# Optimization experiments

Hardware: AMD Instinct MI355X
Metric: run time of the kernel (lower is better)

## Reference

```python
import jax, jax.numpy as jnp
import numpy as np

V, E, H = 2048, 256, 256
B, T, MMAX = 256, 16, 96  # blocks, max tokens/instr, max instrs/block


def setup_inputs() -> dict:
    key = jax.random.key(0)
    ks = jax.random.split(key, 13)
    # instruction lengths sorted descending (enforce_sorted=True), 96 down to 33
    instr_lens = (96 - (np.arange(B) * 64) // B).astype(np.int64)
    boundaries = np.concatenate([[0], np.cumsum(instr_lens)]).astype(np.int64)
    N = int(boundaries[-1])  # total instructions = 16512
    padded_tokens = jax.random.randint(ks[0], (N, T), 1, V)
    token_lengths = jax.random.randint(ks[1], (N,), 1, T + 1)
    tmask = jnp.arange(T)[None, :] < token_lengths[:, None]
    padded_tokens = jnp.where(tmask, padded_tokens, 0)  # pad with padding_idx=0
    s = 1.0 / np.sqrt(H)
    def u(k, shape):
        return jax.random.uniform(k, shape, jnp.float32, -s, s)
    emb = u(ks[2], (V, E)).at[0].set(0.0)  # padding_idx row is zero
    return dict(
        padded_tokens=padded_tokens.astype(jnp.int64),
        token_lengths=token_lengths.astype(jnp.int64),
        instruction_lengths=jnp.asarray(instr_lens),
        instr_boundaries=jnp.asarray(boundaries),
        embedding=emb,
        w_ih_tok=u(ks[3], (4 * H, E)), w_hh_tok=u(ks[4], (4 * H, H)),
        b_ih_tok=u(ks[5], (4 * H,)), b_hh_tok=u(ks[6], (4 * H,)),
        w_ih_ins=u(ks[7], (4 * H, H)), w_hh_ins=u(ks[8], (4 * H, H)),
        b_ih_ins=u(ks[9], (4 * H,)), b_hh_ins=u(ks[10], (4 * H,)),
        w_lin=u(ks[11], (1, H)), b_lin=u(ks[12], (1,)),
    )


def _lstm_final(x, lengths, w_ih, w_hh, b_ih, b_hh):
    # x: [N, S, D] padded; returns hidden state at last valid step per sequence [N, H]
    N, S, _ = x.shape
    Hh = w_hh.shape[1]
    mask = jnp.arange(S)[:, None] < lengths[None, :]  # [S, N]
    bias = b_ih + b_hh

    def step(carry, inp):
        h, c = carry
        x_t, m = inp  # x_t: [N, D], m: [N]
        g = x_t @ w_ih.T + h @ w_hh.T + bias  # [N, 4H], PyTorch gate order i,f,g,o
        i, f, gg, o = jnp.split(g, 4, axis=-1)
        c_new = jax.nn.sigmoid(f) * c + jax.nn.sigmoid(i) * jnp.tanh(gg)
        h_new = jax.nn.sigmoid(o) * jnp.tanh(c_new)
        m = m[:, None]
        return (jnp.where(m, h_new, h), jnp.where(m, c_new, c)), None

    h0 = jnp.zeros((N, Hh), x.dtype)
    (h, _), _ = jax.lax.scan(step, (h0, h0), (jnp.swapaxes(x, 0, 1), mask))
    return h


def reference(padded_tokens, token_lengths, instruction_lengths, instr_boundaries,
              embedding, w_ih_tok, w_hh_tok, b_ih_tok, b_hh_tok,
              w_ih_ins, w_hh_ins, b_ih_ins, b_hh_ins, w_lin, b_lin):
    # token-level LSTM over all instructions (packed == masked scan)
    emb_tokens = embedding[padded_tokens]  # [N, T, E]
    instr_inputs = _lstm_final(emb_tokens, token_lengths,
                               w_ih_tok, w_hh_tok, b_ih_tok, b_hh_tok)  # [N, H]
    N = instr_inputs.shape[0]
    # regroup instructions into blocks via boundaries (pad_sequence equivalent)
    idx = instr_boundaries[:-1, None] + jnp.arange(MMAX)[None, :]  # [B, MMAX]
    valid = jnp.arange(MMAX)[None, :] < instruction_lengths[:, None]
    gathered = jnp.where(valid[..., None],
                         instr_inputs[jnp.clip(idx, 0, N - 1)], 0.0)  # [B, MMAX, H]
    final = _lstm_final(gathered, instruction_lengths,
                        w_ih_ins, w_hh_ins, b_ih_ins, b_hh_ins)  # [B, H]
    return (final @ w_lin.T + b_lin).squeeze(-1)  # [B]
```

## Files before the change

### kernel.cpp

```cpp
#include <hip/hip_runtime.h>
#include <hip/hip_bf16.h>
#include <math.h>

#define VSZ 2048
#define EDIM 256
#define HDIM 256
#define G4 1024
#define TMAX 16
#define IB 16

typedef _Float16 f16x2 __attribute__((ext_vector_type(2)));
typedef _Float16 f16x4 __attribute__((ext_vector_type(4)));
typedef _Float16 f16x8 __attribute__((ext_vector_type(8)));
typedef float f32x4 __attribute__((ext_vector_type(4)));

#define HA_STRIDE 264
#define GWH_STRIDE 264

__device__ __forceinline__ float fexp2(float x) {
#if defined(__has_builtin) && __has_builtin(__builtin_amdgcn_exp2f)
  return __builtin_amdgcn_exp2f(x);
#else
  return exp2f(x);
#endif
}
__device__ __forceinline__ float frcp(float x) {
#if defined(__has_builtin) && __has_builtin(__builtin_amdgcn_rcpf)
  return __builtin_amdgcn_rcpf(x);
#else
  return 1.0f / x;
#endif
}
__device__ __forceinline__ float sigm(float x) {
  return frcp(1.0f + fexp2(x * -1.44269504f));
}
__device__ __forceinline__ float tanh_fast(float x) {
  float t = fexp2(fminf(x, 15.0f) * 2.88539008f);
  return (t - 1.0f) * frcp(t + 1.0f);
}

__device__ __forceinline__ float fdot2(f16x2 a, f16x2 b, float c) {
#if defined(__has_builtin) && __has_builtin(__builtin_amdgcn_fdot2)
  return __builtin_amdgcn_fdot2(a, b, c, false);
#else
  return c + (float)a.x * (float)b.x + (float)a.y * (float)b.y;
#endif
}

__device__ __forceinline__ float dot8h(uint4 w, float4 hv, float acc) {
  f16x2 h0 = __builtin_bit_cast(f16x2, hv.x);
  f16x2 h1 = __builtin_bit_cast(f16x2, hv.y);
  f16x2 h2 = __builtin_bit_cast(f16x2, hv.z);
  f16x2 h3 = __builtin_bit_cast(f16x2, hv.w);
  f16x2 w0 = __builtin_bit_cast(f16x2, w.x);
  f16x2 w1 = __builtin_bit_cast(f16x2, w.y);
  f16x2 w2 = __builtin_bit_cast(f16x2, w.z);
  f16x2 w3 = __builtin_bit_cast(f16x2, w.w);
  return fdot2(h3, w3, fdot2(h2, w2, fdot2(h1, w1, fdot2(h0, w0, acc))));
}

__device__ __forceinline__ bool is_f32(const void* w) {
  const unsigned short* p = (const unsigned short*)w;
  int pl = 0;
#pragma unroll
  for (int i = 0; i < 64; ++i) {
    unsigned e = (p[2 * i] >> 7) & 0xFF;
    pl += (e >= 113 && e <= 122) ? 1 : 0;
  }
  return pl < 48;
}

template <bool F32>
__device__ __forceinline__ float ldf(const void* p, long j) {
  if (F32) return ((const float*)p)[j];
  return __uint_as_float(((unsigned)((const unsigned short*)p)[j]) << 16);
}
__device__ __forceinline__ float ldf_rt(const void* p, long j, bool f32) {
  if (f32) return ((const float*)p)[j];
  return __uint_as_float(((unsigned)((const unsigned short*)p)[j]) << 16);
}
template <bool I64>
__device__ __forceinline__ int ldi(const int* p, int j) {
  return I64 ? p[2 * j] : p[j];
}
__device__ __forceinline__ int ldi_rt(const int* p, int j, bool i64) {
  return i64 ? p[2 * j] : p[j];
}

__global__ __launch_bounds__(256) void k_transp(const void* src, float* __restrict__ dst,
                                                const void* fprobe) {
  __shared__ float tile[32][33];
  __shared__ int sf;
  if (threadIdx.x == 0) sf = is_f32(fprobe) ? 1 : 0;
  __syncthreads();
  const bool f32 = (sf != 0);
  const int tx = threadIdx.x & 31, ty = threadIdx.x >> 5;
  const int r0 = blockIdx.x * 32, c0 = blockIdx.y * 32;
#pragma unroll
  for (int q = 0; q < 4; ++q) {
    int rr = ty + q * 8;
    tile[rr][tx] = ldf_rt(src, (long)(r0 + rr) * 256 + (c0 + tx), f32);
  }
  __syncthreads();
#pragma unroll
  for (int q = 0; q < 4; ++q) {
    int cc = ty + q * 8;
    dst[(size_t)(c0 + cc) * 1024 + (r0 + tx)] = tile[tx][cc];
  }
}

__global__ __launch_bounds__(256) void k_pack(const void* src, uint4* __restrict__ dst,
                                              const void* fprobe) {
  __shared__ int sf;
  if (threadIdx.x == 0) sf = is_f32(fprobe) ? 1 : 0;
  __syncthreads();
  const bool f32 = (sf != 0);
  const int idx = blockIdx.x * 256 + threadIdx.x;
  const int rr = idx & 255, j = (idx >> 8) & 3, c = idx >> 10;
  const long base = (long)(j * 256 + rr) * 256 + 8 * c;
  unsigned u[4];
#pragma unroll
  for (int q = 0; q < 4; ++q) {
    f16x2 v;
    v.x = (_Float16)ldf_rt(src, base + 2 * q, f32);
    v.y = (_Float16)ldf_rt(src, base + 2 * q + 1, f32);
    u[q] = __builtin_bit_cast(unsigned, v);
  }
  uint4 o; o.x = u[0]; o.y = u[1]; o.z = u[2]; o.w = u[3];
  dst[idx] = o;
}

__global__ __launch_bounds__(256) void k_packB(const void* src, f16x8* __restrict__ dst,
                                               const void* fprobe) {
  __shared__ int sf;
  if (threadIdx.x == 0) sf = is_f32(fprobe) ? 1 : 0;
  __syncthreads();
  const bool f32 = (sf != 0);
  const int idx = blockIdx.x * 256 + threadIdx.x;
  const int l = idx & 63;
  int rest = idx >> 6;
  const int kt = rest & 7; rest >>= 3;
  const int nt = rest & 15;
  const int w = rest >> 4;
  const int n = 256 * w + nt * 16 + (l & 15);
  const int j = n & 3, e = n >> 2;
  const long base = (long)(j * 256 + e) * 256 + kt * 32 + ((l >> 4) << 3);
  f16x8 v;
#pragma unroll
  for (int q = 0; q < 8; ++q) v[q] = (_Float16)ldf_rt(src, base + q, f32);
  dst[idx] = v;
}

template <bool F32>
__device__ void tok_table_impl(const void* emb, const float* __restrict__ wT,
                               const void* bih, const void* bhh,
                               f16x4* __restrict__ tabi4, float (*xs)[256]) {
  const int t = threadIdx.x;
  const int v0 = blockIdx.x * 16;
#pragma unroll
  for (int i = 0; i < 16; ++i) xs[i][t] = ldf<F32>(emb, (long)(v0 + i) * EDIM + t);
  __syncthreads();
  float acc[4][16];
#pragma unroll
  for (int j = 0; j < 4; ++j)
#pragma unroll
    for (int i = 0; i < 16; ++i) acc[j][i] = 0.f;
  for (int k4 = 0; k4 < 64; ++k4) {
    float w[4][4];
#pragma unroll
    for (int kk = 0; kk < 4; ++kk)
#pragma unroll
      for (int j = 0; j < 4; ++j)
        w[j][kk] = wT[(size_t)(k4 * 4 + kk) * 1024 + j * 256 + t];
#pragma unroll
    for (int i = 0; i < 16; ++i) {
      float4 h4 = *(const float4*)&xs[i][k4 * 4];
#pragma unroll
      for (int j = 0; j < 4; ++j)
        acc[j][i] = fmaf(h4.x, w[j][0], fmaf(h4.y, w[j][1],
                    fmaf(h4.z, w[j][2], fmaf(h4.w, w[j][3], acc[j][i]))));
    }
  }
  float b[4];
#pragma unroll
  for (int j = 0; j < 4; ++j)
    b[j] = ldf<F32>(bih, j * 256 + t) + ldf<F32>(bhh, j * 256 + t);
#pragma unroll
  for (int i = 0; i < 16; ++i) {
    f16x4 v;
    v.x = (_Float16)(acc[0][i] + b[0]);
    v.y = (_Float16)(acc[1][i] + b[1]);
    v.z = (_Float16)(acc[2][i] + b[2]);
    v.w = (_Float16)(acc[3][i] + b[3]);
    tabi4[(size_t)(v0 + i) * 256 + t] = v;
  }
}

__global__ __launch_bounds__(256) void k_tok_table(
    const void* emb, const float* __restrict__ wT, const void* bih,
    const void* bhh, f16x4* __restrict__ tabi4, const void* fprobe) {
  __shared__ float xs[16][256];
  __shared__ int sf;
  if (threadIdx.x == 0) sf = is_f32(fprobe) ? 1 : 0;
  __syncthreads();
  if (sf) tok_table_impl<true>(emb, wT, bih, bhh, tabi4, xs);
  else    tok_table_impl<false>(emb, wT, bih, bhh, tabi4, xs);
}

__global__ __launch_bounds__(1024) void k_bucket(const int* tlen, int N,
                                                 int* __restrict__ perm,
                                                 const int* iprobe) {
  __shared__ int cnt[16][18];
  __shared__ int wbase[16][18];
  __shared__ int base[18];
  const int t = threadIdx.x;
  const int w = t >> 6;
  const bool i64 = (iprobe[1] == 0);
  if (t < 16 * 18) ((int*)cnt)[t] = 0;
  __syncthreads();
  for (int n = t; n < N; n += 1024) {
    int len = ldi_rt(tlen, n, i64);
    len = max(0, min(16, len));
    atomicAdd(&cnt[w][len], 1);
  }
  __syncthreads();
  if (t < 17) {
    int s = 0;
    for (int ww = 0; ww < 16; ++ww) { wbase[ww][t] = s; s += cnt[ww][t]; }
    base[t] = s;
  }
  __syncthreads();
  if (t == 0) {
    int s = 0;
    for (int i = 0; i <= 16; ++i) { int c = base[i]; base[i] = s; s += c; }
  }
  __syncthreads();
  if (t < 16 * 18) ((int*)cnt)[t] = 0;
  __syncthreads();
  for (int n = t; n < N; n += 1024) {
    int len = ldi_rt(tlen, n, i64);
    len = max(0, min(16, len));
    int pos = base[len] + wbase[w][len] + atomicAdd(&cnt[w][len], 1);
    perm[pos] = n;
  }
}

struct TokSmemM {
  _Float16 gateW[4][16 * GWH_STRIDE];
  _Float16 hA[16 * HA_STRIDE];
  int tokL[IB][TMAX];
  int lenL[IB];
  int nIdx[IB];
};

template <bool I64>
__device__ void tok_mfma_impl(const int* tok32, const int* tlen32,
                              const int* __restrict__ perm,
                              const f16x4* __restrict__ tabi4,
                              const f16x8* __restrict__ pkB,
                              const f16x8* __restrict__ pkBI,
                              const void* bihI, const void* bhhI,
                              float* __restrict__ instrH, float* __restrict__ gx,
                              int N, int do_gx, bool f32, TokSmemM& sm) {
  const int n0 = blockIdx.x * IB, t = threadIdx.x;
  const int w = t >> 6, l = t & 63;
  if (t < IB) {
    int slot = n0 + t;
    int n = (slot < N) ? perm[slot] : -1;
    sm.nIdx[t] = n;
    sm.lenL[t] = (n >= 0) ? ldi<I64>(tlen32, n) : 0;
  }
  for (int idx = t; idx < 16 * HA_STRIDE / 2; idx += 256) ((unsigned*)sm.hA)[idx] = 0;
  __syncthreads();
  {
    int i = t >> 4, s = t & 15;
    int n = sm.nIdx[i];
    sm.tokL[i][s] = (n >= 0) ? ldi<I64>(tok32, n * TMAX + s) : 0;
  }
  float c[IB];
#pragma unroll
  for (int i = 0; i < IB; ++i) c[i] = 0.f;
  __syncthreads();
  int maxlen = 0;
#pragma unroll
  for (int i = 0; i < IB; ++i) maxlen = max(maxlen, sm.lenL[i]);

  const f16x8* Bp = pkB + (size_t)w * (16 * 8 * 64);
  const int aOff = (l & 15) * HA_STRIDE + ((l >> 4) << 3);
  const int m0 = (l >> 4) << 2;
  _Float16* gw = sm.gateW[w];

  for (int s = 0; s < maxlen; ++s) {
    f16x8 aF[8];
#pragma unroll
    for (int kt = 0; kt < 8; ++kt)
      aF[kt] = *(const f16x8*)&sm.hA[aOff + kt * 32];
#pragma unroll 2
    for (int g4 = 0; g4 < 4; ++g4) {
      f32x4 a0 = {0.f, 0.f, 0.f, 0.f}, a1 = a0, a2 = a0, a3 = a0;
#pragma unroll
      for (int kt = 0; kt < 8; ++kt) {
        const f16x8* bb = Bp + ((size_t)(g4 * 4) * 8 + kt) * 64 + l;
        f16x8 b0 = bb[0 * 8 * 64];
        f16x8 b1 = bb[1 * 8 * 64];
        f16x8 b2 = bb[2 * 8 * 64];
        f16x8 b3 = bb[3 * 8 * 64];
        a0 = __builtin_amdgcn_mfma_f32_16x16x32_f16(aF[kt], b0, a0, 0, 0, 0);
        a1 = __builtin_amdgcn_mfma_f32_16x16x32_f16(aF[kt], b1, a1, 0, 0, 0);
        a2 = __builtin_amdgcn_mfma_f32_16x16x32_f16(aF[kt], b2, a2, 0, 0, 0);
        a3 = __builtin_amdgcn_mfma_f32_16x16x32_f16(aF[kt], b3, a3, 0, 0, 0);
      }
      const int colb = (l & 15);
#pragma unroll
      for (int r = 0; r < 4; ++r) {
        gw[(m0 + r) * GWH_STRIDE + (g4 * 4 + 0) * 16 + colb] = (_Float16)a0[r];
        gw[(m0 + r) * GWH_STRIDE + (g4 * 4 + 1) * 16 + colb] = (_Float16)a1[r];
        gw[(m0 + r) * GWH_STRIDE + (g4 * 4 + 2) * 16 + colb] = (_Float16)a2[r];
        gw[(m0 + r) * GWH_STRIDE + (g4 * 4 + 3) * 16 + colb] = (_Float16)a3[r];
      }
    }
    __syncthreads();
#pragma unroll
    for (int m = 0; m < IB; ++m) {
      if (s < sm.lenL[m]) {
        f16x4 gv = *(const f16x4*)&gw[m * GWH_STRIDE + 4 * l];
        f16x4 tb = tabi4[(size_t)sm.tokL[m][s] * 256 + t];
        float gi = (float)gv.x + (float)tb.x;
        float gf = (float)gv.y + (float)tb.y;
        float gg = (float)gv.z + (float)tb.z;
        float go = (float)gv.w + (float)tb.w;
        float si = sigm(gi), sf = sigm(gf), tg = tanh_fast(gg), so = sigm(go);
        c[m] = sf * c[m] + si * tg;
        sm.hA[m * HA_STRIDE + t] = (_Float16)(so * tanh_fast(c[m]));
      }
    }
    __syncthreads();
  }
#pragma unroll
  for (int m = 0; m < IB; ++m) {
    int n = sm.nIdx[m];
    if (n >= 0) instrH[(size_t)n * HDIM + t] = (float)sm.hA[m * HA_STRIDE + t];
  }
  if (do_gx) {
    f16x8 aF[8];
#pragma unroll
    for (int kt = 0; kt < 8; ++kt)
      aF[kt] = *(const f16x8*)&sm.hA[aOff + kt * 32];
    const f16x8* BpI = pkBI + (size_t)w * (16 * 8 * 64);
#pragma unroll 2
    for (int g4 = 0; g4 < 4; ++g4) {
      f32x4 a0 = {0.f, 0.f, 0.f, 0.f}, a1 = a0, a2 = a0, a3 = a0;
#pragma unroll
      for (int kt = 0; kt < 8; ++kt) {
        const f16x8* bb = BpI + ((size_t)(g4 * 4) * 8 + kt) * 64 + l;
        f16x8 b0 = bb[0 * 8 * 64];
        f16x8 b1 = bb[1 * 8 * 64];
        f16x8 b2 = bb[2 * 8 * 64];
        f16x8 b3 = bb[3 * 8 * 64];
        a0 = __builtin_amdgcn_mfma_f32_16x16x32_f16(aF[kt], b0, a0, 0, 0, 0);
        a1 = __builtin_amdgcn_mfma_f32_16x16x32_f16(aF[kt], b1, a1, 0, 0, 0);
        a2 = __builtin_amdgcn_mfma_f32_16x16x32_f16(aF[kt], b2, a2, 0, 0, 0);
        a3 = __builtin_amdgcn_mfma_f32_16x16x32_f16(aF[kt], b3, a3, 0, 0, 0);
      }
      const int colb = (l & 15);
#pragma unroll
      for (int r = 0; r < 4; ++r) {
        gw[(m0 + r) * GWH_STRIDE + (g4 * 4 + 0) * 16 + colb] = (_Float16)a0[r];
        gw[(m0 + r) * GWH_STRIDE + (g4 * 4 + 1) * 16 + colb] = (_Float16)a1[r];
        gw[(m0 + r) * GWH_STRIDE + (g4 * 4 + 2) * 16 + colb] = (_Float16)a2[r];
        gw[(m0 + r) * GWH_STRIDE + (g4 * 4 + 3) * 16 + colb] = (_Float16)a3[r];
      }
    }
    __syncthreads();
    const float bj0 = ldf_rt(bihI, 0 * 256 + t, f32) + ldf_rt(bhhI, 0 * 256 + t, f32);
    const float bj1 = ldf_rt(bihI, 1 * 256 + t, f32) + ldf_rt(bhhI, 1 * 256 + t, f32);
    const float bj2 = ldf_rt(bihI, 2 * 256 + t, f32) + ldf_rt(bhhI, 2 * 256 + t, f32);
    const float bj3 = ldf_rt(bihI, 3 * 256 + t, f32) + ldf_rt(bhhI, 3 * 256 + t, f32);
#pragma unroll
    for (int m = 0; m < IB; ++m) {
      int n = sm.nIdx[m];
      if (n >= 0) {
        f16x4 gv = *(const f16x4*)&gw[m * GWH_STRIDE + 4 * l];
        gx[(size_t)n * G4 +       t] = (float)gv.x + bj0;
        gx[(size_t)n * G4 + 256 + t] = (float)gv.y + bj1;
        gx[(size_t)n * G4 + 512 + t] = (float)gv.z + bj2;
        gx[(size_t)n * G4 + 768 + t] = (float)gv.w + bj3;
      }
    }
  }
}

__global__ __launch_bounds__(256, 2) void k_tok_lstm(
    const int* tok32, const int* tlen32, const int* __restrict__ perm,
    const f16x4* __restrict__ tabi4, const f16x8* __restrict__ pkB,
    const f16x8* __restrict__ pkBI, const void* bihI, const void* bhhI,
    float* __restrict__ instrH, float* __restrict__ gx, int N, int do_gx,
    const int* iprobe, const void* fprobe) {
  __shared__ TokSmemM sm;
  __shared__ int sfl;
  if (threadIdx.x == 0)
    sfl = ((iprobe[1] == 0) ? 1 : 0) | (is_f32(fprobe) ? 2 : 0);
  __syncthreads();
  const bool f32 = (sfl & 2) != 0;
  if (sfl & 1) tok_mfma_impl<true >(tok32, tlen32, perm, tabi4, pkB, pkBI, bihI, bhhI, instrH, gx, N, do_gx, f32, sm);
  else         tok_mfma_impl<false>(tok32, tlen32, perm, tabi4, pkB, pkBI, bihI, bhhI, instrH, gx, N, do_gx, f32, sm);
}

#define RCH 24
#define LCH 8
struct InsSmem {
  uint4 wL[LCH][1024];
  float gL[1024];
  f16x2 hL2[128];
  float red[256];
};

template <bool F32, bool I64>
__device__ void ins_rec_impl(const int* ilen32, const int* bnd32,
                             const float* __restrict__ gx,
                             const uint4* __restrict__ pk,
                             const void* wlin, const void* blin,
                             float* __restrict__ out, int B, InsSmem& sm) {
  const int b = blockIdx.x, t = threadIdx.x;
  const int j = t >> 8, rr = t & 255;
  const int len = ldi<I64>(ilen32, b);
  const long n0 = (long)ldi<I64>(bnd32, b);
#pragma unroll
  for (int cc = 0; cc < LCH; ++cc)
    sm.wL[cc][t] = pk[((RCH + cc) * 4 + j) * 256 + rr];
  uint4 wr[RCH];
#pragma unroll
  for (int cg = 0; cg < RCH; ++cg)
    wr[cg] = pk[(cg * 4 + j) * 256 + rr];
  if (t < 128) {
    f16x2 z; z.x = (_Float16)0.f; z.y = (_Float16)0.f;
    sm.hL2[t] = z;
  }
  float c = 0.f, h = 0.f;
  __syncthreads();

  for (int m = 0; m < len; ++m) {
    float g0 = 0.f, g1 = 0.f, g2 = 0.f, g3 = 0.f;
    if (t < 256) {
      const float* gp = gx + (size_t)(n0 + m) * G4;
      g0 = gp[t]; g1 = gp[256 + t]; g2 = gp[512 + t]; g3 = gp[768 + t];
    }
    float a0 = 0.f, a1 = 0.f;
#pragma unroll
    for (int cg = 0; cg < RCH; ++cg) {
      float4 hv = ((const float4*)sm.hL2)[cg];
      if (cg & 1) a1 = dot8h(wr[cg], hv, a1);
      else        a0 = dot8h(wr[cg], hv, a0);
    }
#pragma unroll
    for (int cc = 0; cc < LCH; ++cc) {
      float4 hv = ((const float4*)sm.hL2)[RCH + cc];
      if (cc & 1) a1 = dot8h(sm.wL[cc][t], hv, a1);
      else        a0 = dot8h(sm.wL[cc][t], hv, a0);
    }
    sm.gL[t] = a0 + a1;
    __syncthreads();
    if (t < 256) {
      float gi = g0 + sm.gL[t];
      float gf = g1 + sm.gL[256 + t];
      float gg = g2 + sm.gL[512 + t];
      float go = g3 + sm.gL[768 + t];
      float si = sigm(gi), sf = sigm(gf), tg = tanh_fast(gg), so = sigm(go);
      c = sf * c + si * tg;
      h = so * tanh_fast(c);
      ((_Float16*)sm.hL2)[t] = (_Float16)h;
    }
    __syncthreads();
  }
  if (t < 256) sm.red[t] = h * ldf<F32>(wlin, t);
  __syncthreads();
  for (int st = 128; st > 0; st >>= 1) {
    if (t < st) sm.red[t] += sm.red[t + st];
    __syncthreads();
  }
  if (t == 0) out[b] = sm.red[0] + ldf<F32>(blin, 0);
}

__global__ __launch_bounds__(1024) void k_ins_rec(
    const int* ilen32, const int* bnd32, const float* __restrict__ gx,
    const uint4* __restrict__ pk, const void* wlin, const void* blin,
    float* __restrict__ out, int B, const void* fprobe, const int* iprobe) {
  __shared__ InsSmem sm;
  __shared__ int sfl;
  if (threadIdx.x == 0)
    sfl = (is_f32(fprobe) ? 1 : 0) | ((iprobe[1] == 0) ? 2 : 0);
  __syncthreads();
  const int fl = sfl;
  if (fl == 0)      ins_rec_impl<false, false>(ilen32, bnd32, gx, pk, wlin, blin, out, B, sm);
  else if (fl == 1) ins_rec_impl<true,  false>(ilen32, bnd32, gx, pk, wlin, blin, out, B, sm);
  else if (fl == 2) ins_rec_impl<false, true >(ilen32, bnd32, gx, pk, wlin, blin, out, B, sm);
  else              ins_rec_impl<true,  true >(ilen32, bnd32, gx, pk, wlin, blin, out, B, sm);
}

#define IBB 4
struct InsSmemFB {
  float hL[IBB][HDIM];
  float xL[IBB][HDIM];
  float gL[IBB][G4];
};

template <bool F32, bool I64>
__device__ void ins_fb_impl(const int* ilen32, const int* bnd32,
                            const float* __restrict__ instrH,
                            const float* __restrict__ wTih,
                            const float* __restrict__ wThh,
                            const void* bih, const void* bhh,
                            const void* wlin, const void* blin,
                            float* __restrict__ out, int B, InsSmemFB& sm) {
  const int wg = blockIdx.x, t = threadIdx.x;
  const int myblk = t >> 8, myelem = t & 255;
  int len[IBB], n0[IBB];
#pragma unroll
  for (int i = 0; i < IBB; ++i) {
    int b = wg * IBB + i;
    len[i] = (b < B) ? ldi<I64>(ilen32, b) : 0;
    n0[i]  = (b < B) ? ldi<I64>(bnd32, b) : 0;
  }
  float c = 0.f;
  sm.hL[myblk][myelem] = 0.f;
  float bias_r = ldf<F32>(bih, t) + ldf<F32>(bhh, t);
  __syncthreads();
  int maxlen = 0;
#pragma unroll
  for (int i = 0; i < IBB; ++i) maxlen = max(maxlen, len[i]);
  for (int m = 0; m < maxlen; ++m) {
    unsigned act = 0;
#pragma unroll
    for (int i = 0; i < IBB; ++i) if (m < len[i]) act |= (1u << i);
    if (m < len[myblk])
      sm.xL[myblk][myelem] = instrH[(size_t)(n0[myblk] + m) * HDIM + myelem];
    __syncthreads();
    float a[IBB];
#pragma unroll
    for (int i = 0; i < IBB; ++i) a[i] = (act & (1u << i)) ? bias_r : 0.f;
    for (int k4 = 0; k4 < 64; ++k4) {
      float w0 = wThh[(size_t)(k4 * 4 + 0) * 1024 + t];
      float w1 = wThh[(size_t)(k4 * 4 + 1) * 1024 + t];
      float w2 = wThh[(size_t)(k4 * 4 + 2) * 1024 + t];
      float w3 = wThh[(size_t)(k4 * 4 + 3) * 1024 + t];
      float u0 = wTih[(size_t)(k4 * 4 + 0) * 1024 + t];
      float u1 = wTih[(size_t)(k4 * 4 + 1) * 1024 + t];
      float u2 = wTih[(size_t)(k4 * 4 + 2) * 1024 + t];
      float u3 = wTih[(size_t)(k4 * 4 + 3) * 1024 + t];
#pragma unroll
      for (int i = 0; i < IBB; ++i) {
        if (!(act & (1u << i))) continue;
        float4 h4 = *(const float4*)&sm.hL[i][k4 * 4];
        float4 x4 = *(const float4*)&sm.xL[i][k4 * 4];
        a[i] = fmaf(h4.x, w0, fmaf(h4.y, w1, fmaf(h4.z, w2, fmaf(h4.w, w3, a[i]))));
        a[i] = fmaf(x4.x, u0, fmaf(x4.y, u1, fmaf(x4.z, u2, fmaf(x4.w, u3, a[i]))));
      }
    }
#pragma unroll
    for (int i = 0; i < IBB; ++i)
      if (act & (1u << i)) sm.gL[i][t] = a[i];
    __syncthreads();
    if (m < len[myblk]) {
      float si = sigm(sm.gL[myblk][myelem]);
      float sf = sigm(sm.gL[myblk][256 + myelem]);
      float tg = tanh_fast(sm.gL[myblk][512 + myelem]);
      float so = sigm(sm.gL[myblk][768 + myelem]);
      c = sf * c + si * tg;
      sm.hL[myblk][myelem] = so * tanh_fast(c);
    }
    __syncthreads();
  }
  sm.gL[myblk][myelem] = sm.hL[myblk][myelem] * ldf<F32>(wlin, myelem);
  __syncthreads();
  for (int st = 128; st > 0; st >>= 1) {
    if (myelem < st) sm.gL[myblk][myelem] += sm.gL[myblk][myelem + st];
    __syncthreads();
  }
  if (myelem == 0 && wg * IBB + myblk < B)
    out[wg * IBB + myblk] = sm.gL[myblk][0] + ldf<F32>(blin, 0);
}

__global__ __launch_bounds__(1024) void k_ins_fb(
    const int* ilen32, const int* bnd32, const float* __restrict__ instrH,
    const float* __restrict__ wTih, const float* __restrict__ wThh,
    const void* bih, const void* bhh, const void* wlin, const void* blin,
    float* __restrict__ out, int B, const void* fprobe, const int* iprobe) {
  __shared__ InsSmemFB sm;
  __shared__ int sfl;
  if (threadIdx.x == 0)
    sfl = (is_f32(fprobe) ? 1 : 0) | ((iprobe[1] == 0) ? 2 : 0);
  __syncthreads();
  const int fl = sfl;
  if (fl == 0)      ins_fb_impl<false, false>(ilen32, bnd32, instrH, wTih, wThh, bih, bhh, wlin, blin, out, B, sm);
  else if (fl == 1) ins_fb_impl<true,  false>(ilen32, bnd32, instrH, wTih, wThh, bih, bhh, wlin, blin, out, B, sm);
  else if (fl == 2) ins_fb_impl<false, true >(ilen32, bnd32, instrH, wTih, wThh, bih, bhh, wlin, blin, out, B, sm);
  else              ins_fb_impl<true,  true >(ilen32, bnd32, instrH, wTih, wThh, bih, bhh, wlin, blin, out, B, sm);
}

extern "C" void kernel_launch(void* const* d_in, const int* in_sizes, int n_in,
                              void* d_out, int out_size, void* d_ws, size_t ws_size,
                              hipStream_t stream) {
  const int N = in_sizes[1];
  const int B = in_sizes[2];

  float* ws = (float*)d_ws;
  size_t off = 0;
  f16x4* tabi4 = (f16x4*)(ws + off); off += (size_t)VSZ * G4 / 2;
  float* instrH   = ws + off; off += (size_t)N * HDIM;
  float* wT_ihI   = ws + off; off += 262144;
  float* wT_hhI   = ws + off; off += 262144;
  float* wT_ihT   = ws + off; off += 262144;
  f16x8* pkB_tok  = (f16x8*)(ws + off); off += 131072;
  f16x8* pkB_ins  = (f16x8*)(ws + off); off += 131072;
  uint4* pk_ins   = (uint4*)(ws + off); off += 131072;
  int*   permI    = (int*)(ws + off);
  off += ((size_t)N + 15) & ~(size_t)15;
  float* gx       = ws + off;
  const size_t need_gx = (off + (size_t)N * G4) * sizeof(float);
  const bool has_gx = (ws_size >= need_gx);

  const void* fprobe = d_in[5];
  const int*  iprobe = (const int*)d_in[1];

  hipLaunchKernelGGL(k_transp, dim3(32, 8), dim3(256), 0, stream, d_in[5], wT_ihT, fprobe);
  hipLaunchKernelGGL(k_transp, dim3(32, 8), dim3(256), 0, stream, d_in[9], wT_ihI, fprobe);
  hipLaunchKernelGGL(k_transp, dim3(32, 8), dim3(256), 0, stream, d_in[10], wT_hhI, fprobe);
  hipLaunchKernelGGL(k_packB, dim3(128), dim3(256), 0, stream, d_in[6], pkB_tok, fprobe);
  hipLaunchKernelGGL(k_packB, dim3(128), dim3(256), 0, stream, d_in[9], pkB_ins, fprobe);
  hipLaunchKernelGGL(k_pack, dim3(128), dim3(256), 0, stream, d_in[10], pk_ins, fprobe);

  hipLaunchKernelGGL(k_tok_table, dim3(VSZ / 16), dim3(256), 0, stream,
                     d_in[4], wT_ihT, d_in[7], d_in[8], tabi4, fprobe);
  hipLaunchKernelGGL(k_bucket, dim3(1), dim3(1024), 0, stream,
                     (const int*)d_in[1], N, permI, iprobe);
  hipLaunchKernelGGL(k_tok_lstm, dim3((N + IB - 1) / IB), dim3(256), 0, stream,
                     (const int*)d_in[0], (const int*)d_in[1], permI, tabi4,
                     pkB_tok, pkB_ins, d_in[11], d_in[12], instrH, gx, N,
                     has_gx ? 1 : 0, iprobe, fprobe);
  if (has_gx) {
    hipLaunchKernelGGL(k_ins_rec, dim3(B), dim3(1024), 0, stream,
                       (const int*)d_in[2], (const int*)d_in[3], gx, pk_ins,
                       d_in[13], d_in[14], (float*)d_out, B, fprobe, iprobe);
  } else {
    hipLaunchKernelGGL(k_ins_fb, dim3((B + IBB - 1) / IBB), dim3(1024), 0, stream,
                       (const int*)d_in[2], (const int*)d_in[3], instrH,
                       wT_ihI, wT_hhI, d_in[11], d_in[12], d_in[13], d_in[14],
                       (float*)d_out, B, fprobe, iprobe);
  }
}
```

Baseline: 688.9 us.

## Make token LSTM gate elementwise wave-local, removing mid-step barrier

Each wave now processes gate outputs for its own 64 hidden units in two 32-wide halves. It applies the LSTM cell update straight from its private gate buffer, so the intra-step __syncthreads between the MFMA and the elementwise phase is no longer needed. The gate scratch buffer shrinks to half-width per wave and token ids are stored as 16-bit, which cuts shared memory use. The cost is that each thread now holds 16 cell states in a different lane mapping. Interleaving the halves with sched_barrier is meant to overlap MFMA and transcendental work, but it may raise register pressure.

Measured after the change: 1.449 ms. 2.1x slower.

```diff
diff --git a/kernel.cpp b/kernel.cpp
--- a/kernel.cpp
+++ b/kernel.cpp
@@ -15,7 +15,7 @@
 typedef float f32x4 __attribute__((ext_vector_type(4)));
 
 #define HA_STRIDE 264
-#define GWH_STRIDE 264
+#define GH_STRIDE 132
 
 __device__ __forceinline__ float fexp2(float x) {
 #if defined(__has_builtin) && __has_builtin(__builtin_amdgcn_exp2f)
@@ -246,9 +246,9 @@
 }
 
 struct TokSmemM {
-  _Float16 gateW[4][16 * GWH_STRIDE];
+  _Float16 gw4[4][16 * GH_STRIDE];
   _Float16 hA[16 * HA_STRIDE];
-  int tokL[IB][TMAX];
+  unsigned short tokL[IB][TMAX];
   int lenL[IB];
   int nIdx[IB];
 };
@@ -275,7 +275,7 @@
   {
     int i = t >> 4, s = t & 15;
     int n = sm.nIdx[i];
-    sm.tokL[i][s] = (n >= 0) ? ldi<I64>(tok32, n * TMAX + s) : 0;
+    sm.tokL[i][s] = (unsigned short)((n >= 0) ? ldi<I64>(tok32, n * TMAX + s) : 0);
   }
   float c[IB];
 #pragma unroll
@@ -288,58 +288,89 @@
   const f16x8* Bp = pkB + (size_t)w * (16 * 8 * 64);
   const int aOff = (l & 15) * HA_STRIDE + ((l >> 4) << 3);
   const int m0 = (l >> 4) << 2;
-  _Float16* gw = sm.gateW[w];
+  const int colb = l & 15;
+  const int eh = l & 31;
+  const int rp = l >> 5;
+  _Float16* gwq = sm.gw4[w];
+
+#define HALF_MFMA(GH, BASEP)                                                          \
+  {                                                                                   \
+    f32x4 a0 = {0.f, 0.f, 0.f, 0.f}, a1 = a0, a2 = a0, a3 = a0;                       \
+    _Pragma("unroll") for (int kt = 0; kt < 8; ++kt) {                                \
+      const f16x8* bb = BASEP + ((size_t)((GH) * 4) * 8 + kt) * 64 + l;               \
+      f16x8 b0 = bb[0 * 8 * 64];                                                      \
+      f16x8 b1 = bb[1 * 8 * 64];                                                      \
+      f16x8 b2 = bb[2 * 8 * 64];                                                      \
+      f16x8 b3 = bb[3 * 8 * 64];                                                      \
+      a0 = __builtin_amdgcn_mfma_f32_16x16x32_f16(aF[kt], b0, a0, 0, 0, 0);           \
+      a1 = __builtin_amdgcn_mfma_f32_16x16x32_f16(aF[kt], b1, a1, 0, 0, 0);           \
+      a2 = __builtin_amdgcn_mfma_f32_16x16x32_f16(aF[kt], b2, a2, 0, 0, 0);           \
+      a3 = __builtin_amdgcn_mfma_f32_16x16x32_f16(aF[kt], b3, a3, 0, 0, 0);           \
+    }                                                                                 \
+    const int cb = ((GH) & 1) * 64 + colb;                                            \
+    _Pragma("unroll") for (int r = 0; r < 4; ++r) {                                   \
+      gwq[(m0 + r) * GH_STRIDE + cb + 0 * 16] = (_Float16)a0[r];                      \
+      gwq[(m0 + r) * GH_STRIDE + cb + 1 * 16] = (_Float16)a1[r];                      \
+      gwq[(m0 + r) * GH_STRIDE + cb + 2 * 16] = (_Float16)a2[r];                      \
+      gwq[(m0 + r) * GH_STRIDE + cb + 3 * 16] = (_Float16)a3[r];                      \
+    }                                                                                 \
+  }
 
   for (int s = 0; s < maxlen; ++s) {
     f16x8 aF[8];
 #pragma unroll
     for (int kt = 0; kt < 8; ++kt)
       aF[kt] = *(const f16x8*)&sm.hA[aOff + kt * 32];
-#pragma unroll 2
-    for (int g4 = 0; g4 < 4; ++g4) {
-      f32x4 a0 = {0.f, 0.f, 0.f, 0.f}, a1 = a0, a2 = a0, a3 = a0;
-#pragma unroll
-      for (int kt = 0; kt < 8; ++kt) {
-        const f16x8* bb = Bp + ((size_t)(g4 * 4) * 8 + kt) * 64 + l;
-        f16x8 b0 = bb[0 * 8 * 64];
-        f16x8 b1 = bb[1 * 8 * 64];
-        f16x8 b2 = bb[2 * 8 * 64];
-        f16x8 b3 = bb[3 * 8 * 64];
-        a0 = __builtin_amdgcn_mfma_f32_16x16x32_f16(aF[kt], b0, a0, 0, 0, 0);
-        a1 = __builtin_amdgcn_mfma_f32_16x16x32_f16(aF[kt], b1, a1, 0, 0, 0);
-        a2 = __builtin_amdgcn_mfma_f32_16x16x32_f16(aF[kt], b2, a2, 0, 0, 0);
-        a3 = __builtin_amdgcn_mfma_f32_16x16x32_f16(aF[kt], b3, a3, 0, 0, 0);
+    __syncthreads();
+    HALF_MFMA(0, Bp)
+    HALF_MFMA(1, Bp)
+    {
+      const int e = 64 * w + eh;
+#pragma unroll
+      for (int i = 0; i < 8; ++i) {
+        const int m = 2 * i + rp;
+        if (s < sm.lenL[m]) {
+          f16x4 gv = *(const f16x4*)&gwq[m * GH_STRIDE + 4 * eh];
+          f16x4 tb = tabi4[(size_t)sm.tokL[m][s] * 256 + e];
+          float gi = (float)gv.x + (float)tb.x;
+          float gf = (float)gv.y + (float)tb.y;
+          float gg = (float)gv.z + (float)tb.z;
+          float go = (float)gv.w + (float)tb.w;
+          float si = sigm(gi), sf = sigm(gf), tg = tanh_fast(gg), so = sigm(go);
+          c[i] = sf * c[i] + si * tg;
+          sm.hA[m * HA_STRIDE + e] = (_Float16)(so * tanh_fast(c[i]));
+        }
       }
-      const int colb = (l & 15);
-#pragma unroll
-      for (int r = 0; r < 4; ++r) {
-        gw[(m0 + r) * GWH_STRIDE + (g4 * 4 + 0) * 16 + colb] = (_Float16)a0[r];
-        gw[(m0 + r) * GWH_STRIDE + (g4 * 4 + 1) * 16 + colb] = (_Float16)a1[r];
-        gw[(m0 + r) * GWH_STRIDE + (g4 * 4 + 2) * 16 + colb] = (_Float16)a2[r];
-        gw[(m0 + r) * GWH_STRIDE + (g4 * 4 + 3) * 16 + colb] = (_Float16)a3[r];
+    }
+    __builtin_amdgcn_sched_barrier(0);
+    HALF_MFMA(2, Bp)
+    HALF_MFMA(3, Bp)
+    {
+      const int e = 64 * w + 32 + eh;
+#pragma unroll
+      for (int i = 0; i < 8; ++i) {
+        const int m = 2 * i + rp;
+        if (s < sm.lenL[m]) {
+          f16x4 gv = *(const f16x4*)&gwq[m * GH_STRIDE + 4 * eh];
+          f16x4 tb = tabi4[(size_t)sm.tokL[m][s] * 256 + e];
+          float gi = (float)gv.x + (float)tb.x;
+          float gf = (float)gv.y + (float)tb.y;
+          float gg = (float)gv.z + (float)tb.z;
+          float go = (float)gv.w + (float)tb.w;
+          float si = sigm(gi), sf = sigm(gf), tg = tanh_fast(gg), so = sigm(go);
+          c[8 + i] = sf * c[8 + i] + si * tg;
+          sm.hA[m * HA_STRIDE + e] = (_Float16)(so * tanh_fast(c[8 + i]));
+        }
       }
     }
     __syncthreads();
+  }
+  if (!do_gx) {
 #pragma unroll
     for (int m = 0; m < IB; ++m) {
-      if (s < sm.lenL[m]) {
-        f16x4 gv = *(const f16x4*)&gw[m * GWH_STRIDE + 4 * l];
-        f16x4 tb = tabi4[(size_t)sm.tokL[m][s] * 256 + t];
-        float gi = (float)gv.x + (float)tb.x;
-        float gf = (float)gv.y + (float)tb.y;
-        float gg = (float)gv.z + (float)tb.z;
-        float go = (float)gv.w + (float)tb.w;
-        float si = sigm(gi), sf = sigm(gf), tg = tanh_fast(gg), so = sigm(go);
-        c[m] = sf * c[m] + si * tg;
-        sm.hA[m * HA_STRIDE + t] = (_Float16)(so * tanh_fast(c[m]));
-      }
-    }
-    __syncthreads();
-  }
-#pragma unroll
-  for (int m = 0; m < IB; ++m) {
-    int n = sm.nIdx[m];
-    if (n >= 0) instrH[(size_t)n * HDIM + t] = (float)sm.hA[m * HA_STRIDE + t];
+      int n = sm.nIdx[m];
+      if (n >= 0) instrH[(size_t)n * HDIM + t] = (float)sm.hA[m * HA_STRIDE + t];
+    }
   }
   if (do_gx) {
     f16x8 aF[8];
@@ -347,47 +378,31 @@
     for (int kt = 0; kt < 8; ++kt)
       aF[kt] = *(const f16x8*)&sm.hA[aOff + kt * 32];
     const f16x8* BpI = pkBI + (size_t)w * (16 * 8 * 64);
-#pragma unroll 2
-    for (int g4 = 0; g4 < 4; ++g4) {
-      f32x4 a0 = {0.f, 0.f, 0.f, 0.f}, a1 = a0, a2 = a0, a3 = a0;
-#pragma unroll
-      for (int kt = 0; kt < 8; ++kt) {
-        const f16x8* bb = BpI + ((size_t)(g4 * 4) * 8 + kt) * 64 + l;
-        f16x8 b0 = bb[0 * 8 * 64];
-        f16x8 b1 = bb[1 * 8 * 64];
-        f16x8 b2 = bb[2 * 8 * 64];
-        f16x8 b3 = bb[3 * 8 * 64];
-        a0 = __builtin_amdgcn_mfma_f32_16x16x32_f16(aF[kt], b0, a0, 0, 0, 0);
-        a1 = __builtin_amdgcn_mfma_f32_16x16x32_f16(aF[kt], b1, a1, 0, 0, 0);
-        a2 = __builtin_amdgcn_mfma_f32_16x16x32_f16(aF[kt], b2, a2, 0, 0, 0);
-        a3 = __builtin_amdgcn_mfma_f32_16x16x32_f16(aF[kt], b3, a3, 0, 0, 0);
+#pragma unroll
+    for (int half = 0; half < 2; ++half) {
+      if (half == 0) { HALF_MFMA(0, BpI) HALF_MFMA(1, BpI) }
+      else           { HALF_MFMA(2, BpI) HALF_MFMA(3, BpI) }
+      const int e = 64 * w + 32 * half + eh;
+      const float bj0 = ldf_rt(bihI, 0 * 256 + e, f32) + ldf_rt(bhhI, 0 * 256 + e, f32);
+      const float bj1 = ldf_rt(bihI, 1 * 256 + e, f32) + ldf_rt(bhhI, 1 * 256 + e, f32);
+      const float bj2 = ldf_rt(bihI, 2 * 256 + e, f32) + ldf_rt(bhhI, 2 * 256 + e, f32);
+      const float bj3 = ldf_rt(bihI, 3 * 256 + e, f32) + ldf_rt(bhhI, 3 * 256 + e, f32);
+#pragma unroll
+      for (int i = 0; i < 8; ++i) {
+        const int m = 2 * i + rp;
+        int n = sm.nIdx[m];
+        if (n >= 0) {
+          f16x4 gv = *(const f16x4*)&gwq[m * GH_STRIDE + 4 * eh];
+          gx[(size_t)n * G4 +       e] = (float)gv.x + bj0;
+          gx[(size_t)n * G4 + 256 + e] = (float)gv.y + bj1;
+          gx[(size_t)n * G4 + 512 + e] = (float)gv.z + bj2;
+          gx[(size_t)n * G4 + 768 + e] = (float)gv.w + bj3;
+        }
       }
-      const int colb = (l & 15);
-#pragma unroll
-      for (int r = 0; r < 4; ++r) {
-        gw[(m0 + r) * GWH_STRIDE + (g4 * 4 + 0) * 16 + colb] = (_Float16)a0[r];
-        gw[(m0 + r) * GWH_STRIDE + (g4 * 4 + 1) * 16 + colb] = (_Float16)a1[r];
-        gw[(m0 + r) * GWH_STRIDE + (g4 * 4 + 2) * 16 + colb] = (_Float16)a2[r];
-        gw[(m0 + r) * GWH_STRIDE + (g4 * 4 + 3) * 16 + colb] = (_Float16)a3[r];
-      }
-    }
-    __syncthreads();
-    const float bj0 = ldf_rt(bihI, 0 * 256 + t, f32) + ldf_rt(bhhI, 0 * 256 + t, f32);
-    const float bj1 = ldf_rt(bihI, 1 * 256 + t, f32) + ldf_rt(bhhI, 1 * 256 + t, f32);
-    const float bj2 = ldf_rt(bihI, 2 * 256 + t, f32) + ldf_rt(bhhI, 2 * 256 + t, f32);
-    const float bj3 = ldf_rt(bihI, 3 * 256 + t, f32) + ldf_rt(bhhI, 3 * 256 + t, f32);
-#pragma unroll
-    for (int m = 0; m < IB; ++m) {
-      int n = sm.nIdx[m];
-      if (n >= 0) {
-        f16x4 gv = *(const f16x4*)&gw[m * GWH_STRIDE + 4 * l];
-        gx[(size_t)n * G4 +       t] = (float)gv.x + bj0;
-        gx[(size_t)n * G4 + 256 + t] = (float)gv.y + bj1;
-        gx[(size_t)n * G4 + 512 + t] = (float)gv.z + bj2;
-        gx[(size_t)n * G4 + 768 + t] = (float)gv.w + bj3;
-      }
-    }
-  }
+      __builtin_amdgcn_sched_barrier(0);
+    }
+  }
+#undef HALF_MFMA
 }
 
 __global__ __launch_bounds__(256, 2) void k_tok_lstm(
```
